# Kernel tuning notes

Hardware: AMD Instinct MI355X
Metric: run time of the kernel (lower is better)

## Reference

```python
import jax, jax.numpy as jnp
import numpy as np

ALPHA = 10.0
BETA = 2.0
NUM_CLASSES = 98
EMB = 512
N = 8192

def l2_normalize(x, axis):
    return x / jnp.linalg.norm(x, axis=axis, keepdims=True)

def setup_inputs() -> dict:
    key = jax.random.key(0)
    k1, k2, k3 = jax.random.split(key, 3)
    inputs = jax.random.normal(k1, (N, EMB), dtype=jnp.float32)
    inputs = l2_normalize(inputs, axis=1)  # embeddings are unit-norm cosine features
    targets = jax.random.randint(k2, (N,), 0, NUM_CLASSES, dtype=jnp.int64)
    # kernel: uniform(-1,1) then renorm columns to tiny norm then scale -> effectively
    # columns get L2-normalized anyway in forward; plain uniform init is faithful.
    kernel = jax.random.uniform(k3, (EMB, NUM_CLASSES), dtype=jnp.float32, minval=-1.0, maxval=1.0)
    return {"inputs": inputs, "targets": targets, "kernel": kernel}

def reference(inputs, targets, kernel):
    n = inputs.shape[0]
    # pairwise similarity [n, n]
    sim_mat = inputs @ inputs.T
    # margin-adjusted logits
    kernel_norm = l2_normalize(kernel, axis=0)
    cos_theta = jnp.clip(inputs @ kernel_norm, -1.0, 1.0)  # [n, C]
    onehot = jax.nn.one_hot(targets, NUM_CLASSES, dtype=jnp.bool_)
    output = jnp.where(onehot, cos_theta - BETA, cos_theta) * ALPHA
    # cross entropy (mean)
    logp = jax.nn.log_softmax(output, axis=1)
    loss = -jnp.mean(jnp.take_along_axis(logp, targets[:, None], axis=1))
    # precision
    pred = jnp.argmax(output, axis=1)
    prec = jnp.mean((pred == targets).astype(jnp.float32))
    # vectorized per-sample masked pos/neg similarity means
    same = targets[:, None] == targets[None, :]           # [n, n]
    pos_mask = same & (sim_mat < 1.0)                     # excludes self (sim == 1)
    neg_mask = ~same
    posf = pos_mask.astype(sim_mat.dtype)
    negf = neg_mask.astype(sim_mat.dtype)
    pos_mean_i = jnp.sum(sim_mat * posf, axis=1) / jnp.sum(posf, axis=1)
    neg_mean_i = jnp.sum(sim_mat * negf, axis=1) / jnp.sum(negf, axis=1)
    mean_pos_sim = jnp.mean(pos_mean_i)
    mean_neg_sim = jnp.mean(neg_mean_i)
    return (loss, prec, mean_pos_sim, mean_neg_sim)
```

## Files before the change

kernel.cpp:

```cpp
#include <hip/hip_runtime.h>
#include <hip/hip_bf16.h>

typedef __attribute__((ext_vector_type(8))) short bf16x8;
typedef __attribute__((ext_vector_type(4))) float f32x4;

#define NROWS 8192
#define EMB   512
#define NCLS  98
#define NCPAD 128
#define MAXPER 256
#define NBLK  (NROWS / 32)
#define ALPHA_F 10.0f
#define BETA_F  2.0f

__device__ __forceinline__ unsigned short f2bf(float x) {
    unsigned u = __builtin_bit_cast(unsigned, x);
    u += 0x7FFF + ((u >> 16) & 1);
    return (unsigned short)(u >> 16);
}

__device__ __forceinline__ void g2l16(const void* g, void* l) {
    __builtin_amdgcn_global_load_lds(
        (const __attribute__((address_space(1))) unsigned int*)g,
        (__attribute__((address_space(3))) unsigned int*)l, 16, 0, 0);
}

__global__ __launch_bounds__(1024) void init_scatter_kernel(
        const int* __restrict__ T, int* __restrict__ cnt, int* __restrict__ bucket,
        unsigned int* __restrict__ ctr, float* __restrict__ usum) {
    __shared__ int lh[NCLS];
    const int tid = threadIdx.x;
    if (tid < NCLS) lh[tid] = 0;
    if (tid == 0) *ctr = 0;
    if (tid < EMB) usum[tid] = 0.f;
    __syncthreads();
    #pragma unroll
    for (int k = 0; k < NROWS / 1024; ++k) {
        int i = k * 1024 + tid;
        int t = T[i];
        int slot = atomicAdd(&lh[t], 1);
        if (slot < MAXPER) bucket[t * MAXPER + slot] = i;
    }
    __syncthreads();
    if (tid < NCLS) cnt[tid] = lh[tid];
}

__global__ __launch_bounds__(256) void classv_kernel(
        const float* __restrict__ X, const float* __restrict__ K,
        const int* __restrict__ cnt, const int* __restrict__ bucket,
        float* __restrict__ V, float* __restrict__ usum,
        unsigned short* __restrict__ KbT) {
    const int tid = threadIdx.x;
    const int lane = tid & 63, w = tid >> 6;
    const int bx = blockIdx.x;

    if (bx >= 784) {
        int c = (bx - 784) * 4 + w;
        if (c < NCLS) {
            float v[8]; float s = 0.f;
            #pragma unroll
            for (int q = 0; q < 8; ++q) {
                float x = K[(size_t)(lane + q * 64) * NCLS + c];
                v[q] = x; s = fmaf(x, x, s);
            }
            #pragma unroll
            for (int d = 32; d > 0; d >>= 1) s += __shfl_xor(s, d);
            float inv = 1.0f / sqrtf(s);
            #pragma unroll
            for (int q = 0; q < 8; ++q)
                KbT[(size_t)c * EMB + lane + q * 64] = f2bf(v[q] * inv);
        } else {
            #pragma unroll
            for (int q = 0; q < 8; ++q)
                KbT[(size_t)c * EMB + lane + q * 64] = 0;
        }
        return;
    }

    __shared__ float red[3][64];
    const int c = bx >> 3, d0 = (bx & 7) * 64;
    int n = cnt[c]; if (n > MAXPER) n = MAXPER;
    const int* bk = bucket + c * MAXPER;
    float a = 0.f;
    for (int j = w; j < n; j += 4) {
        int row = bk[j];
        a += X[(size_t)row * EMB + d0 + lane];
    }
    if (w > 0) red[w - 1][lane] = a;
    __syncthreads();
    if (w == 0) {
        a += red[0][lane] + red[1][lane] + red[2][lane];
        V[(size_t)c * EMB + d0 + lane] = a;
        atomicAdd(&usum[d0 + lane], a);
    }
}

__global__ __launch_bounds__(256) void main_gemm(
        const float* __restrict__ X, const unsigned short* __restrict__ KbT,
        const int* __restrict__ T, const int* __restrict__ cnt,
        const float* __restrict__ V, const float* __restrict__ usum,
        double* __restrict__ partials, unsigned int* __restrict__ ctr,
        float* __restrict__ out) {
    __shared__ unsigned short As[32 * 64];
    __shared__ unsigned short Bs[NCPAD * 64];
    __shared__ float P[32][NCPAD];
    __shared__ int   trow[32];
    __shared__ double redacc[4][4];
    __shared__ int   lastflag;

    const int tid = threadIdx.x;
    const int w = tid >> 6, lane = tid & 63;
    const int row0 = blockIdx.x * 32;
    const int wr = w & 1, wc = w >> 1;
    const int c0 = lane & 15, g = lane >> 4;

    const int ar = tid >> 3, ak = (tid & 7) * 8;
    const int myt = T[row0 + ar];
    if (tid < 32) trow[tid] = T[row0 + tid];
    const float* vrow = V + (size_t)myt * EMB;

    float s = 0.f, sm = 0.f; double d = 0.0;
    f32x4 av[4] = {};
    for (int kk = 0; kk < EMB; kk += 64) {
        const float* xp = X + (size_t)(row0 + ar) * EMB + kk + ak;
        float4 xa0 = *(const float4*)xp, xa1 = *(const float4*)(xp + 4);
        const float* up = usum + kk + ak;
        float4 ua0 = *(const float4*)up, ua1 = *(const float4*)(up + 4);
        const float* vp = vrow + kk + ak;
        float4 va0 = *(const float4*)vp, va1 = *(const float4*)(vp + 4);
        float xf[8] = {xa0.x, xa0.y, xa0.z, xa0.w, xa1.x, xa1.y, xa1.z, xa1.w};
        float uf[8] = {ua0.x, ua0.y, ua0.z, ua0.w, ua1.x, ua1.y, ua1.z, ua1.w};
        float vf[8] = {va0.x, va0.y, va0.z, va0.w, va1.x, va1.y, va1.z, va1.w};
        bf16x8 areg;
        #pragma unroll
        for (int q = 0; q < 8; ++q) {
            s  = fmaf(xf[q], uf[q], s);
            sm = fmaf(xf[q], vf[q], sm);
            d  = fma((double)xf[q], (double)xf[q], d);
            areg[q] = (short)f2bf(xf[q]);
        }
        __syncthreads();
        *(bf16x8*)&As[ar * 64 + ak] = areg;
        #pragma unroll
        for (int q = 0; q < 4; ++q) {
            int lb = q * 4096 + tid * 16;
            int c = lb >> 7, kb = lb & 127;
            g2l16((const char*)KbT + (size_t)c * 1024 + kk * 2 + kb, (char*)Bs + lb);
        }
        __syncthreads();
        #pragma unroll
        for (int ks = 0; ks < 2; ++ks) {
            bf16x8 a = *(const bf16x8*)&As[(wr * 16 + c0) * 64 + ks * 32 + g * 8];
            #pragma unroll
            for (int ni = 0; ni < 4; ++ni) {
                bf16x8 b = *(const bf16x8*)&Bs[(wc * 64 + ni * 16 + c0) * 64 + ks * 32 + g * 8];
                av[ni] = __builtin_amdgcn_mfma_f32_16x16x32_bf16(a, b, av[ni], 0, 0, 0);
            }
        }
    }

    #pragma unroll
    for (int m = 1; m < 8; m <<= 1) {
        s += __shfl_xor(s, m); sm += __shfl_xor(sm, m); d += __shfl_xor(d, m);
    }
    double pc = 0.0, nc = 0.0;
    if ((lane & 7) == 0) {
        int h = cnt[myt];
        float pos_sum; int pos_cnt;
        if (d < 1.0) { pos_sum = sm;            pos_cnt = h;     }
        else         { pos_sum = sm - (float)d; pos_cnt = h - 1; }
        float neg_sum = s - sm;
        pc = (double)(pos_sum / (float)pos_cnt);
        nc = (double)(neg_sum / (float)(NROWS - h));
    }
    #pragma unroll
    for (int m = 1; m < 64; m <<= 1) { pc += __shfl_xor(pc, m); nc += __shfl_xor(nc, m); }

    __syncthreads();
    #pragma unroll
    for (int ni = 0; ni < 4; ++ni)
        #pragma unroll
        for (int r = 0; r < 4; ++r)
            P[wr * 16 + g * 4 + r][wc * 64 + ni * 16 + c0] = av[ni][r];
    __syncthreads();

    float lossacc = 0.f, pracc = 0.f;
    #pragma unroll
    for (int j = 0; j < 8; ++j) {
        const int rl = w * 8 + j;
        const int tgt = trow[rl];
        float l1 = P[rl][lane], l2 = P[rl][lane + 64];
        {
            float cos1 = fminf(1.f, fmaxf(-1.f, l1));
            float cos2 = fminf(1.f, fmaxf(-1.f, l2));
            l1 = (cos1 - (lane == tgt ? BETA_F : 0.f)) * ALPHA_F;
            l2 = (cos2 - (lane + 64 == tgt ? BETA_F : 0.f)) * ALPHA_F;
            if (lane      >= NCLS) l1 = -1e30f;
            if (lane + 64 >= NCLS) l2 = -1e30f;
        }
        float m = fmaxf(l1, l2);
        #pragma unroll
        for (int dd = 1; dd < 64; dd <<= 1) m = fmaxf(m, __shfl_xor(m, dd));
        float se = (lane < NCLS ? __expf(l1 - m) : 0.f)
                 + (lane + 64 < NCLS ? __expf(l2 - m) : 0.f);
        float tval = (lane == tgt) ? l1 : ((lane + 64 == tgt) ? l2 : -1e30f);
        float bv; int bi;
        if (l2 > l1) { bv = l2; bi = lane + 64; } else { bv = l1; bi = lane; }
        #pragma unroll
        for (int dd = 1; dd < 64; dd <<= 1) {
            se += __shfl_xor(se, dd);
            tval = fmaxf(tval, __shfl_xor(tval, dd));
            float ov = __shfl_xor(bv, dd); int oi = __shfl_xor(bi, dd);
            if (ov > bv || (ov == bv && oi < bi)) { bv = ov; bi = oi; }
        }
        lossacc += (m + logf(se)) - tval;
        pracc   += (bi == tgt) ? 1.f : 0.f;
    }

    if (lane == 0) {
        redacc[w][0] = (double)lossacc;
        redacc[w][1] = (double)pracc;
        redacc[w][2] = pc;
        redacc[w][3] = nc;
    }
    __syncthreads();
    if (tid == 0) {
        const int bx = blockIdx.x;
        partials[bx * 4 + 0] = redacc[0][0] + redacc[1][0] + redacc[2][0] + redacc[3][0];
        partials[bx * 4 + 1] = redacc[0][1] + redacc[1][1] + redacc[2][1] + redacc[3][1];
        partials[bx * 4 + 2] = redacc[0][2] + redacc[1][2] + redacc[2][2] + redacc[3][2];
        partials[bx * 4 + 3] = redacc[0][3] + redacc[1][3] + redacc[2][3] + redacc[3][3];
        __threadfence();
        lastflag = (atomicAdd(ctr, 1u) == NBLK - 1) ? 1 : 0;
    }
    __syncthreads();
    if (lastflag && w == 0) {
        __threadfence();
        double a0 = 0.0, a1 = 0.0, a2 = 0.0, a3 = 0.0;
        for (int i = lane; i < NBLK; i += 64) {
            a0 += partials[i * 4 + 0];
            a1 += partials[i * 4 + 1];
            a2 += partials[i * 4 + 2];
            a3 += partials[i * 4 + 3];
        }
        #pragma unroll
        for (int m = 1; m < 64; m <<= 1) {
            a0 += __shfl_xor(a0, m); a1 += __shfl_xor(a1, m);
            a2 += __shfl_xor(a2, m); a3 += __shfl_xor(a3, m);
        }
        if (lane == 0) {
            out[0] = (float)(a0 / NROWS);
            out[1] = (float)(a1 / NROWS);
            out[2] = (float)(a2 / NROWS);
            out[3] = (float)(a3 / NROWS);
        }
    }
}

#define BM 64
#define BN 64
#define BK 32
#define LDA 68

__global__ void hist_kernel(const int* __restrict__ t, int* __restrict__ hist) {
    int i = blockIdx.x * blockDim.x + threadIdx.x;
    if (i < NROWS) atomicAdd(&hist[t[i]], 1);
}

__global__ void colnorm_kernel(const float* __restrict__ K, float* __restrict__ colinv) {
    int c = blockIdx.x;
    float s = 0.f;
    for (int k = threadIdx.x; k < EMB; k += 64) {
        float v = K[k * NCLS + c];
        s = fmaf(v, v, s);
    }
    #pragma unroll
    for (int off = 32; off > 0; off >>= 1) s += __shfl_down(s, off);
    if (threadIdx.x == 0) colinv[c] = 1.0f / sqrtf(s);
}

__global__ __launch_bounds__(256) void simred_kernel(
        const float* __restrict__ X, const int* __restrict__ T,
        float* __restrict__ S, float* __restrict__ SAME) {
    __shared__ float As[BK * LDA];
    __shared__ float Bs[BK * LDA];
    __shared__ int   trow[BM], tcol[BN];
    __shared__ float redS[BM], redSame[BM];

    const int tid = threadIdx.x;
    const int tx = tid & 15, ty = tid >> 4;
    const int i0 = blockIdx.x * BM, j0 = blockIdx.y * BN;

    if (tid < BM) {
        trow[tid] = T[i0 + tid];
        tcol[tid] = T[j0 + tid];
        redS[tid] = 0.f;
        redSame[tid] = 0.f;
    }

    float c[4][4] = {};
    for (int kk = 0; kk < EMB; kk += BK) {
        #pragma unroll
        for (int q = 0; q < 2; ++q) {
            int l  = tid * 2 + q;
            int r  = l >> 3;
            int kq = (l & 7) << 2;
            const float4 va = *(const float4*)(X + (size_t)(i0 + r) * EMB + kk + kq);
            As[(kq + 0) * LDA + r] = va.x;
            As[(kq + 1) * LDA + r] = va.y;
            As[(kq + 2) * LDA + r] = va.z;
            As[(kq + 3) * LDA + r] = va.w;
            const float4 vb = *(const float4*)(X + (size_t)(j0 + r) * EMB + kk + kq);
            Bs[(kq + 0) * LDA + r] = vb.x;
            Bs[(kq + 1) * LDA + r] = vb.y;
            Bs[(kq + 2) * LDA + r] = vb.z;
            Bs[(kq + 3) * LDA + r] = vb.w;
        }
        __syncthreads();
        #pragma unroll
        for (int k = 0; k < BK; ++k) {
            float4 a4 = *(const float4*)&As[k * LDA + ty * 4];
            float4 b4 = *(const float4*)&Bs[k * LDA + tx * 4];
            float a[4] = {a4.x, a4.y, a4.z, a4.w};
            float b[4] = {b4.x, b4.y, b4.z, b4.w};
            #pragma unroll
            for (int i = 0; i < 4; ++i)
                #pragma unroll
                for (int j = 0; j < 4; ++j)
                    c[i][j] = fmaf(a[i], b[j], c[i][j]);
        }
        __syncthreads();
    }

    #pragma unroll
    for (int i = 0; i < 4; ++i) {
        int r = ty * 4 + i;
        int tr = trow[r];
        float s = 0.f, sm = 0.f;
        #pragma unroll
        for (int j = 0; j < 4; ++j) {
            float v = c[i][j];
            s += v;
            if (tcol[tx * 4 + j] == tr) sm += v;
        }
        atomicAdd(&redS[r], s);
        atomicAdd(&redSame[r], sm);
    }
    __syncthreads();
    if (tid < BM) {
        atomicAdd(&S[i0 + tid],    redS[tid]);
        atomicAdd(&SAME[i0 + tid], redSame[tid]);
    }
}

__global__ __launch_bounds__(128) void loss_kernel(
        const float* __restrict__ X, const int* __restrict__ T,
        const float* __restrict__ K, const float* __restrict__ colinv,
        double* __restrict__ acc) {
    const int row = blockIdx.x;
    const int tid = threadIdx.x;
    __shared__ float xs[EMB];
    *(float4*)&xs[tid * 4] = *(const float4*)&X[(size_t)row * EMB + tid * 4];
    __syncthreads();

    const int tgt = T[row];
    const int c = tid;
    float logit = -1e30f;
    if (c < NCLS) {
        float d = 0.f;
        #pragma unroll 4
        for (int k = 0; k < EMB; ++k) d = fmaf(K[k * NCLS + c], xs[k], d);
        float cosv = d * colinv[c];
        cosv = fminf(1.f, fmaxf(-1.f, cosv));
        logit = (cosv - (c == tgt ? BETA_F : 0.f)) * ALPHA_F;
    }

    __shared__ float rv[128];
    __shared__ int   ri[128];
    __shared__ float Lt;
    if (c == tgt) Lt = logit;

    rv[tid] = logit;
    __syncthreads();
    #pragma unroll
    for (int s = 64; s > 0; s >>= 1) {
        if (tid < s) rv[tid] = fmaxf(rv[tid], rv[tid + s]);
        __syncthreads();
    }
    const float m = rv[0];
    __syncthreads();

    rv[tid] = (c < NCLS) ? expf(logit - m) : 0.f;
    __syncthreads();
    #pragma unroll
    for (int s = 64; s > 0; s >>= 1) {
        if (tid < s) rv[tid] += rv[tid + s];
        __syncthreads();
    }
    const float lse = m + logf(rv[0]);
    __syncthreads();

    rv[tid] = logit;
    ri[tid] = (c < NCLS) ? c : 0x7fffffff;
    __syncthreads();
    #pragma unroll
    for (int s = 64; s > 0; s >>= 1) {
        if (tid < s) {
            float vo = rv[tid + s]; int io = ri[tid + s];
            if (vo > rv[tid] || (vo == rv[tid] && io < ri[tid])) { rv[tid] = vo; ri[tid] = io; }
        }
        __syncthreads();
    }

    if (tid == 0) {
        float loss_i = lse - Lt;
        atomicAdd(&acc[0], (double)loss_i);
        atomicAdd(&acc[1], (ri[0] == tgt) ? 1.0 : 0.0);
    }
}

__global__ void finalize_kernel(
        const float* __restrict__ X, const int* __restrict__ T,
        const int* __restrict__ hist, const float* __restrict__ S,
        const float* __restrict__ SAME, double* __restrict__ acc) {
    int r = blockIdx.x * blockDim.x + threadIdx.x;
    if (r >= NROWS) return;
    const float* x = X + (size_t)r * EMB;
    double d = 0.0;
    for (int k = 0; k < EMB; ++k) d = fma((double)x[k], (double)x[k], d);
    int h = hist[T[r]];
    float same = SAME[r];
    float pos_sum; int pos_cnt;
    if (d < 1.0) { pos_sum = same;            pos_cnt = h;     }
    else         { pos_sum = same - (float)d; pos_cnt = h - 1; }
    float neg_sum = S[r] - same;
    int   neg_cnt = NROWS - h;
    atomicAdd(&acc[2], (double)(pos_sum / (float)pos_cnt));
    atomicAdd(&acc[3], (double)(neg_sum / (float)neg_cnt));
}

__global__ void out_kernel(const double* __restrict__ acc, float* __restrict__ out) {
    if (threadIdx.x == 0) {
        out[0] = (float)(acc[0] / NROWS);
        out[1] = (float)(acc[1] / NROWS);
        out[2] = (float)(acc[2] / NROWS);
        out[3] = (float)(acc[3] / NROWS);
    }
}

extern "C" void kernel_launch(void* const* d_in, const int* in_sizes, int n_in,
                              void* d_out, int out_size, void* d_ws, size_t ws_size,
                              hipStream_t stream) {
    const float* X = (const float*)d_in[0];
    const int*   T = (const int*)d_in[1];
    const float* K = (const float*)d_in[2];
    float* out = (float*)d_out;

    const size_t KBT_BYTES    = (size_t)NCPAD * EMB * sizeof(unsigned short);
    const size_t V_BYTES      = (size_t)NCLS * EMB * sizeof(float);
    const size_t BUCKET_BYTES = (size_t)NCLS * MAXPER * sizeof(int);
    const size_t PART_BYTES   = (size_t)NBLK * 4 * sizeof(double);
    const size_t MISC_BYTES   = 128 * sizeof(int) + 64 + 512 * sizeof(float);

    if (ws_size >= KBT_BYTES + V_BYTES + BUCKET_BYTES + PART_BYTES + MISC_BYTES + 256) {
        unsigned short* KbT = (unsigned short*)d_ws;
        float*  V        = (float*)((char*)d_ws + KBT_BYTES);
        int*    bucket   = (int*)((char*)d_ws + KBT_BYTES + V_BYTES);
        double* partials = (double*)((char*)d_ws + KBT_BYTES + V_BYTES + BUCKET_BYTES);
        int*    cnt      = (int*)((char*)partials + PART_BYTES);
        unsigned int* ctr = (unsigned int*)(cnt + 128);
        float*  usum     = (float*)(ctr + 16);

        init_scatter_kernel<<<1, 1024, 0, stream>>>(T, cnt, bucket, ctr, usum);
        classv_kernel<<<816, 256, 0, stream>>>(X, K, cnt, bucket, V, usum, KbT);
        main_gemm<<<NBLK, 256, 0, stream>>>(X, KbT, T, cnt, V, usum, partials, ctr, out);
    } else {
        const size_t FB_BYTES = sizeof(double) * 4 + sizeof(int) * NCLS
                              + sizeof(float) * (NCLS + 2 * NROWS);
        double* acc    = (double*)d_ws;
        int*    hist   = (int*)(acc + 4);
        float*  colinv = (float*)(hist + NCLS);
        float*  S      = colinv + NCLS;
        float*  SAME   = S + NROWS;

        hipMemsetAsync(d_ws, 0, FB_BYTES, stream);
        hist_kernel<<<(NROWS + 255) / 256, 256, 0, stream>>>(T, hist);
        colnorm_kernel<<<NCLS, 64, 0, stream>>>(K, colinv);
        simred_kernel<<<dim3(NROWS / BM, NROWS / BN), 256, 0, stream>>>(X, T, S, SAME);
        loss_kernel<<<NROWS, 128, 0, stream>>>(X, T, K, colinv, acc);
        finalize_kernel<<<(NROWS + 255) / 256, 256, 0, stream>>>(X, T, hist, S, SAME, acc);
        out_kernel<<<1, 64, 0, stream>>>(acc, out);
    }
}
```

Before: 50.18 us.

## Fuse three-kernel pipeline into one cooperative kernel with grid syncs

Replaces the init/scatter, class-vector and main GEMM launches with a single cooperative mega-kernel of 256 blocks that separates its phases with grid.sync(). Init, column normalisation and bucket scatter now run in parallel across blocks instead of in one 1024-thread block. The aim is to remove launch overhead and inter-kernel gaps; in exchange it adds grid-wide barrier costs and relies on cooperative launch, falling back to the old path if that fails. The naive fallback path for a small workspace is removed.

```diff
diff --git a/kernel.cpp b/kernel.cpp
--- a/kernel.cpp
+++ b/kernel.cpp
@@ -1,5 +1,8 @@
 #include <hip/hip_runtime.h>
 #include <hip/hip_bf16.h>
+#include <hip/hip_cooperative_groups.h>
+
+namespace cg = cooperative_groups;
 
 typedef __attribute__((ext_vector_type(8))) short bf16x8;
 typedef __attribute__((ext_vector_type(4))) float f32x4;
@@ -9,7 +12,7 @@
 #define NCLS  98
 #define NCPAD 128
 #define MAXPER 256
-#define NBLK  (NROWS / 32)
+#define NBLK  256
 #define ALPHA_F 10.0f
 #define BETA_F  2.0f
 
@@ -23,6 +26,226 @@
     __builtin_amdgcn_global_load_lds(
         (const __attribute__((address_space(1))) unsigned int*)g,
         (__attribute__((address_space(3))) unsigned int*)l, 16, 0, 0);
+}
+
+__global__ __launch_bounds__(256) void mega_kernel(
+        const float* __restrict__ X, const int* __restrict__ T,
+        const float* __restrict__ K,
+        int* __restrict__ cnt, int* __restrict__ bucket,
+        float* __restrict__ V, float* __restrict__ usum,
+        unsigned short* __restrict__ KbT,
+        double* __restrict__ partials, float* __restrict__ out) {
+    cg::grid_group grid = cg::this_grid();
+
+    __shared__ unsigned short As[32 * 64];
+    __shared__ unsigned short Bs[NCPAD * 64];
+    __shared__ float P[32][NCPAD];
+    __shared__ float redB[3][64];
+    __shared__ int   trow[32];
+    __shared__ double redacc[4][4];
+
+    const int bx = blockIdx.x;
+    const int tid = threadIdx.x;
+    const int w = tid >> 6, lane = tid & 63;
+
+    if (bx == 0) {
+        if (tid < NCLS) cnt[tid] = 0;
+    } else if (bx == 1) {
+        usum[tid] = 0.f; usum[tid + 256] = 0.f;
+    } else if (bx >= 2 && bx < 34) {
+        int c = (bx - 2) * 4 + w;
+        if (c < NCLS) {
+            float v[8]; float s = 0.f;
+            #pragma unroll
+            for (int q = 0; q < 8; ++q) {
+                float x = K[(size_t)(lane + q * 64) * NCLS + c];
+                v[q] = x; s = fmaf(x, x, s);
+            }
+            #pragma unroll
+            for (int d = 32; d > 0; d >>= 1) s += __shfl_xor(s, d);
+            float inv = 1.0f / sqrtf(s);
+            #pragma unroll
+            for (int q = 0; q < 8; ++q)
+                KbT[(size_t)c * EMB + lane + q * 64] = f2bf(v[q] * inv);
+        } else {
+            #pragma unroll
+            for (int q = 0; q < 8; ++q)
+                KbT[(size_t)c * EMB + lane + q * 64] = 0;
+        }
+    }
+    grid.sync();
+
+    if (bx < 32) {
+        int i = bx * 256 + tid;
+        int t = T[i];
+        int slot = atomicAdd(&cnt[t], 1);
+        if (slot < MAXPER) bucket[t * MAXPER + slot] = i;
+    }
+    grid.sync();
+
+    for (int vb = bx; vb < 784; vb += NBLK) {
+        const int c = vb >> 3, d0 = (vb & 7) * 64;
+        int n = cnt[c]; if (n > MAXPER) n = MAXPER;
+        const int* bk = bucket + c * MAXPER;
+        float a = 0.f;
+        for (int j = w; j < n; j += 4) {
+            int row = bk[j];
+            a += X[(size_t)row * EMB + d0 + lane];
+        }
+        if (w > 0) redB[w - 1][lane] = a;
+        __syncthreads();
+        if (w == 0) {
+            a += redB[0][lane] + redB[1][lane] + redB[2][lane];
+            V[(size_t)c * EMB + d0 + lane] = a;
+            atomicAdd(&usum[d0 + lane], a);
+        }
+        __syncthreads();
+    }
+    grid.sync();
+
+    {
+        const int row0 = bx * 32;
+        const int wr = w & 1, wc = w >> 1;
+        const int c0 = lane & 15, g = lane >> 4;
+        const int ar = tid >> 3, ak = (tid & 7) * 8;
+        const int myt = T[row0 + ar];
+        if (tid < 32) trow[tid] = T[row0 + tid];
+        const float* vrow = V + (size_t)myt * EMB;
+
+        float s = 0.f, sm = 0.f; double d = 0.0;
+        f32x4 av[4] = {};
+        for (int kk = 0; kk < EMB; kk += 64) {
+            const float* xp = X + (size_t)(row0 + ar) * EMB + kk + ak;
+            float4 xa0 = *(const float4*)xp, xa1 = *(const float4*)(xp + 4);
+            const float* up = usum + kk + ak;
+            float4 ua0 = *(const float4*)up, ua1 = *(const float4*)(up + 4);
+            const float* vp = vrow + kk + ak;
+            float4 va0 = *(const float4*)vp, va1 = *(const float4*)(vp + 4);
+            float xf[8] = {xa0.x, xa0.y, xa0.z, xa0.w, xa1.x, xa1.y, xa1.z, xa1.w};
+            float uf[8] = {ua0.x, ua0.y, ua0.z, ua0.w, ua1.x, ua1.y, ua1.z, ua1.w};
+            float vf[8] = {va0.x, va0.y, va0.z, va0.w, va1.x, va1.y, va1.z, va1.w};
+            bf16x8 areg;
+            #pragma unroll
+            for (int q = 0; q < 8; ++q) {
+                s  = fmaf(xf[q], uf[q], s);
+                sm = fmaf(xf[q], vf[q], sm);
+                d  = fma((double)xf[q], (double)xf[q], d);
+                areg[q] = (short)f2bf(xf[q]);
+            }
+            __syncthreads();
+            *(bf16x8*)&As[ar * 64 + ak] = areg;
+            #pragma unroll
+            for (int q = 0; q < 4; ++q) {
+                int lb = q * 4096 + tid * 16;
+                int c = lb >> 7, kb = lb & 127;
+                g2l16((const char*)KbT + (size_t)c * 1024 + kk * 2 + kb, (char*)Bs + lb);
+            }
+            __syncthreads();
+            #pragma unroll
+            for (int ks = 0; ks < 2; ++ks) {
+                bf16x8 a = *(const bf16x8*)&As[(wr * 16 + c0) * 64 + ks * 32 + g * 8];
+                #pragma unroll
+                for (int ni = 0; ni < 4; ++ni) {
+                    bf16x8 b = *(const bf16x8*)&Bs[(wc * 64 + ni * 16 + c0) * 64 + ks * 32 + g * 8];
+                    av[ni] = __builtin_amdgcn_mfma_f32_16x16x32_bf16(a, b, av[ni], 0, 0, 0);
+                }
+            }
+        }
+
+        #pragma unroll
+        for (int m = 1; m < 8; m <<= 1) {
+            s += __shfl_xor(s, m); sm += __shfl_xor(sm, m); d += __shfl_xor(d, m);
+        }
+        double pc = 0.0, nc = 0.0;
+        if ((lane & 7) == 0) {
+            int h = cnt[myt];
+            float pos_sum; int pos_cnt;
+            if (d < 1.0) { pos_sum = sm;            pos_cnt = h;     }
+            else         { pos_sum = sm - (float)d; pos_cnt = h - 1; }
+            float neg_sum = s - sm;
+            pc = (double)(pos_sum / (float)pos_cnt);
+            nc = (double)(neg_sum / (float)(NROWS - h));
+        }
+        #pragma unroll
+        for (int m = 1; m < 64; m <<= 1) { pc += __shfl_xor(pc, m); nc += __shfl_xor(nc, m); }
+
+        __syncthreads();
+        #pragma unroll
+        for (int ni = 0; ni < 4; ++ni)
+            #pragma unroll
+            for (int r = 0; r < 4; ++r)
+                P[wr * 16 + g * 4 + r][wc * 64 + ni * 16 + c0] = av[ni][r];
+        __syncthreads();
+
+        float lossacc = 0.f, pracc = 0.f;
+        #pragma unroll
+        for (int j = 0; j < 8; ++j) {
+            const int rl = w * 8 + j;
+            const int tgt = trow[rl];
+            float l1 = P[rl][lane], l2 = P[rl][lane + 64];
+            {
+                float cos1 = fminf(1.f, fmaxf(-1.f, l1));
+                float cos2 = fminf(1.f, fmaxf(-1.f, l2));
+                l1 = (cos1 - (lane == tgt ? BETA_F : 0.f)) * ALPHA_F;
+                l2 = (cos2 - (lane + 64 == tgt ? BETA_F : 0.f)) * ALPHA_F;
+                if (lane      >= NCLS) l1 = -1e30f;
+                if (lane + 64 >= NCLS) l2 = -1e30f;
+            }
+            float m = fmaxf(l1, l2);
+            #pragma unroll
+            for (int dd = 1; dd < 64; dd <<= 1) m = fmaxf(m, __shfl_xor(m, dd));
+            float se = (lane < NCLS ? __expf(l1 - m) : 0.f)
+                     + (lane + 64 < NCLS ? __expf(l2 - m) : 0.f);
+            float tval = (lane == tgt) ? l1 : ((lane + 64 == tgt) ? l2 : -1e30f);
+            float bv; int bi;
+            if (l2 > l1) { bv = l2; bi = lane + 64; } else { bv = l1; bi = lane; }
+            #pragma unroll
+            for (int dd = 1; dd < 64; dd <<= 1) {
+                se += __shfl_xor(se, dd);
+                tval = fmaxf(tval, __shfl_xor(tval, dd));
+                float ov = __shfl_xor(bv, dd); int oi = __shfl_xor(bi, dd);
+                if (ov > bv || (ov == bv && oi < bi)) { bv = ov; bi = oi; }
+            }
+            lossacc += (m + logf(se)) - tval;
+            pracc   += (bi == tgt) ? 1.f : 0.f;
+        }
+
+        if (lane == 0) {
+            redacc[w][0] = (double)lossacc;
+            redacc[w][1] = (double)pracc;
+            redacc[w][2] = pc;
+            redacc[w][3] = nc;
+        }
+        __syncthreads();
+        if (tid == 0) {
+            partials[bx * 4 + 0] = redacc[0][0] + redacc[1][0] + redacc[2][0] + redacc[3][0];
+            partials[bx * 4 + 1] = redacc[0][1] + redacc[1][1] + redacc[2][1] + redacc[3][1];
+            partials[bx * 4 + 2] = redacc[0][2] + redacc[1][2] + redacc[2][2] + redacc[3][2];
+            partials[bx * 4 + 3] = redacc[0][3] + redacc[1][3] + redacc[2][3] + redacc[3][3];
+        }
+    }
+    grid.sync();
+
+    if (bx == 0 && w == 0) {
+        double a0 = 0.0, a1 = 0.0, a2 = 0.0, a3 = 0.0;
+        for (int i = lane; i < NBLK; i += 64) {
+            a0 += partials[i * 4 + 0];
+            a1 += partials[i * 4 + 1];
+            a2 += partials[i * 4 + 2];
+            a3 += partials[i * 4 + 3];
+        }
+        #pragma unroll
+        for (int m = 1; m < 64; m <<= 1) {
+            a0 += __shfl_xor(a0, m); a1 += __shfl_xor(a1, m);
+            a2 += __shfl_xor(a2, m); a3 += __shfl_xor(a3, m);
+        }
+        if (lane == 0) {
+            out[0] = (float)(a0 / NROWS);
+            out[1] = (float)(a1 / NROWS);
+            out[2] = (float)(a2 / NROWS);
+            out[3] = (float)(a3 / NROWS);
+        }
+    }
 }
 
 __global__ __launch_bounds__(1024) void init_scatter_kernel(
@@ -257,197 +480,6 @@
     }
 }
 
-#define BM 64
-#define BN 64
-#define BK 32
-#define LDA 68
-
-__global__ void hist_kernel(const int* __restrict__ t, int* __restrict__ hist) {
-    int i = blockIdx.x * blockDim.x + threadIdx.x;
-    if (i < NROWS) atomicAdd(&hist[t[i]], 1);
-}
-
-__global__ void colnorm_kernel(const float* __restrict__ K, float* __restrict__ colinv) {
-    int c = blockIdx.x;
-    float s = 0.f;
-    for (int k = threadIdx.x; k < EMB; k += 64) {
-        float v = K[k * NCLS + c];
-        s = fmaf(v, v, s);
-    }
-    #pragma unroll
-    for (int off = 32; off > 0; off >>= 1) s += __shfl_down(s, off);
-    if (threadIdx.x == 0) colinv[c] = 1.0f / sqrtf(s);
-}
-
-__global__ __launch_bounds__(256) void simred_kernel(
-        const float* __restrict__ X, const int* __restrict__ T,
-        float* __restrict__ S, float* __restrict__ SAME) {
-    __shared__ float As[BK * LDA];
-    __shared__ float Bs[BK * LDA];
-    __shared__ int   trow[BM], tcol[BN];
-    __shared__ float redS[BM], redSame[BM];
-
-    const int tid = threadIdx.x;
-    const int tx = tid & 15, ty = tid >> 4;
-    const int i0 = blockIdx.x * BM, j0 = blockIdx.y * BN;
-
-    if (tid < BM) {
-        trow[tid] = T[i0 + tid];
-        tcol[tid] = T[j0 + tid];
-        redS[tid] = 0.f;
-        redSame[tid] = 0.f;
-    }
-
-    float c[4][4] = {};
-    for (int kk = 0; kk < EMB; kk += BK) {
-        #pragma unroll
-        for (int q = 0; q < 2; ++q) {
-            int l  = tid * 2 + q;
-            int r  = l >> 3;
-            int kq = (l & 7) << 2;
-            const float4 va = *(const float4*)(X + (size_t)(i0 + r) * EMB + kk + kq);
-            As[(kq + 0) * LDA + r] = va.x;
-            As[(kq + 1) * LDA + r] = va.y;
-            As[(kq + 2) * LDA + r] = va.z;
-            As[(kq + 3) * LDA + r] = va.w;
-            const float4 vb = *(const float4*)(X + (size_t)(j0 + r) * EMB + kk + kq);
-            Bs[(kq + 0) * LDA + r] = vb.x;
-            Bs[(kq + 1) * LDA + r] = vb.y;
-            Bs[(kq + 2) * LDA + r] = vb.z;
-            Bs[(kq + 3) * LDA + r] = vb.w;
-        }
-        __syncthreads();
-        #pragma unroll
-        for (int k = 0; k < BK; ++k) {
-            float4 a4 = *(const float4*)&As[k * LDA + ty * 4];
-            float4 b4 = *(const float4*)&Bs[k * LDA + tx * 4];
-            float a[4] = {a4.x, a4.y, a4.z, a4.w};
-            float b[4] = {b4.x, b4.y, b4.z, b4.w};
-            #pragma unroll
-            for (int i = 0; i < 4; ++i)
-                #pragma unroll
-                for (int j = 0; j < 4; ++j)
-                    c[i][j] = fmaf(a[i], b[j], c[i][j]);
-        }
-        __syncthreads();
-    }
-
-    #pragma unroll
-    for (int i = 0; i < 4; ++i) {
-        int r = ty * 4 + i;
-        int tr = trow[r];
-        float s = 0.f, sm = 0.f;
-        #pragma unroll
-        for (int j = 0; j < 4; ++j) {
-            float v = c[i][j];
-            s += v;
-            if (tcol[tx * 4 + j] == tr) sm += v;
-        }
-        atomicAdd(&redS[r], s);
-        atomicAdd(&redSame[r], sm);
-    }
-    __syncthreads();
-    if (tid < BM) {
-        atomicAdd(&S[i0 + tid],    redS[tid]);
-        atomicAdd(&SAME[i0 + tid], redSame[tid]);
-    }
-}
-
-__global__ __launch_bounds__(128) void loss_kernel(
-        const float* __restrict__ X, const int* __restrict__ T,
-        const float* __restrict__ K, const float* __restrict__ colinv,
-        double* __restrict__ acc) {
-    const int row = blockIdx.x;
-    const int tid = threadIdx.x;
-    __shared__ float xs[EMB];
-    *(float4*)&xs[tid * 4] = *(const float4*)&X[(size_t)row * EMB + tid * 4];
-    __syncthreads();
-
-    const int tgt = T[row];
-    const int c = tid;
-    float logit = -1e30f;
-    if (c < NCLS) {
-        float d = 0.f;
-        #pragma unroll 4
-        for (int k = 0; k < EMB; ++k) d = fmaf(K[k * NCLS + c], xs[k], d);
-        float cosv = d * colinv[c];
-        cosv = fminf(1.f, fmaxf(-1.f, cosv));
-        logit = (cosv - (c == tgt ? BETA_F : 0.f)) * ALPHA_F;
-    }
-
-    __shared__ float rv[128];
-    __shared__ int   ri[128];
-    __shared__ float Lt;
-    if (c == tgt) Lt = logit;
-
-    rv[tid] = logit;
-    __syncthreads();
-    #pragma unroll
-    for (int s = 64; s > 0; s >>= 1) {
-        if (tid < s) rv[tid] = fmaxf(rv[tid], rv[tid + s]);
-        __syncthreads();
-    }
-    const float m = rv[0];
-    __syncthreads();
-
-    rv[tid] = (c < NCLS) ? expf(logit - m) : 0.f;
-    __syncthreads();
-    #pragma unroll
-    for (int s = 64; s > 0; s >>= 1) {
-        if (tid < s) rv[tid] += rv[tid + s];
-        __syncthreads();
-    }
-    const float lse = m + logf(rv[0]);
-    __syncthreads();
-
-    rv[tid] = logit;
-    ri[tid] = (c < NCLS) ? c : 0x7fffffff;
-    __syncthreads();
-    #pragma unroll
-    for (int s = 64; s > 0; s >>= 1) {
-        if (tid < s) {
-            float vo = rv[tid + s]; int io = ri[tid + s];
-            if (vo > rv[tid] || (vo == rv[tid] && io < ri[tid])) { rv[tid] = vo; ri[tid] = io; }
-        }
-        __syncthreads();
-    }
-
-    if (tid == 0) {
-        float loss_i = lse - Lt;
-        atomicAdd(&acc[0], (double)loss_i);
-        atomicAdd(&acc[1], (ri[0] == tgt) ? 1.0 : 0.0);
-    }
-}
-
-__global__ void finalize_kernel(
-        const float* __restrict__ X, const int* __restrict__ T,
-        const int* __restrict__ hist, const float* __restrict__ S,
-        const float* __restrict__ SAME, double* __restrict__ acc) {
-    int r = blockIdx.x * blockDim.x + threadIdx.x;
-    if (r >= NROWS) return;
-    const float* x = X + (size_t)r * EMB;
-    double d = 0.0;
-    for (int k = 0; k < EMB; ++k) d = fma((double)x[k], (double)x[k], d);
-    int h = hist[T[r]];
-    float same = SAME[r];
-    float pos_sum; int pos_cnt;
-    if (d < 1.0) { pos_sum = same;            pos_cnt = h;     }
-    else         { pos_sum = same - (float)d; pos_cnt = h - 1; }
-    float neg_sum = S[r] - same;
-    int   neg_cnt = NROWS - h;
-    atomicAdd(&acc[2], (double)(pos_sum / (float)pos_cnt));
-    atomicAdd(&acc[3], (double)(neg_sum / (float)neg_cnt));
-}
-
-__global__ void out_kernel(const double* __restrict__ acc, float* __restrict__ out) {
-    if (threadIdx.x == 0) {
-        out[0] = (float)(acc[0] / NROWS);
-        out[1] = (float)(acc[1] / NROWS);
-        out[2] = (float)(acc[2] / NROWS);
-        out[3] = (float)(acc[3] / NROWS);
-    }
-}
-
 extern "C" void kernel_launch(void* const* d_in, const int* in_sizes, int n_in,
                               void* d_out, int out_size, void* d_ws, size_t ws_size,
                               hipStream_t stream) {
@@ -462,33 +494,23 @@
     const size_t PART_BYTES   = (size_t)NBLK * 4 * sizeof(double);
     const size_t MISC_BYTES   = 128 * sizeof(int) + 64 + 512 * sizeof(float);
 
-    if (ws_size >= KBT_BYTES + V_BYTES + BUCKET_BYTES + PART_BYTES + MISC_BYTES + 256) {
-        unsigned short* KbT = (unsigned short*)d_ws;
-        float*  V        = (float*)((char*)d_ws + KBT_BYTES);
-        int*    bucket   = (int*)((char*)d_ws + KBT_BYTES + V_BYTES);
-        double* partials = (double*)((char*)d_ws + KBT_BYTES + V_BYTES + BUCKET_BYTES);
-        int*    cnt      = (int*)((char*)partials + PART_BYTES);
-        unsigned int* ctr = (unsigned int*)(cnt + 128);
-        float*  usum     = (float*)(ctr + 16);
-
+    unsigned short* KbT = (unsigned short*)d_ws;
+    float*  V        = (float*)((char*)d_ws + KBT_BYTES);
+    int*    bucket   = (int*)((char*)d_ws + KBT_BYTES + V_BYTES);
+    double* partials = (double*)((char*)d_ws + KBT_BYTES + V_BYTES + BUCKET_BYTES);
+    int*    cnt      = (int*)((char*)partials + PART_BYTES);
+    unsigned int* ctr = (unsigned int*)(cnt + 128);
+    float*  usum     = (float*)(ctr + 16);
+
+    const float* Xa = X; const int* Ta = T; const float* Ka = K;
+    void* args[] = { (void*)&Xa, (void*)&Ta, (void*)&Ka,
+                     (void*)&cnt, (void*)&bucket, (void*)&V, (void*)&usum,
+                     (void*)&KbT, (void*)&partials, (void*)&out };
+    hipError_t err = hipLaunchCooperativeKernel(
+        (const void*)mega_kernel, dim3(NBLK), dim3(256), args, 0, stream);
+    if (err != hipSuccess) {
         init_scatter_kernel<<<1, 1024, 0, stream>>>(T, cnt, bucket, ctr, usum);
         classv_kernel<<<816, 256, 0, stream>>>(X, K, cnt, bucket, V, usum, KbT);
         main_gemm<<<NBLK, 256, 0, stream>>>(X, KbT, T, cnt, V, usum, partials, ctr, out);
-    } else {
-        const size_t FB_BYTES = sizeof(double) * 4 + sizeof(int) * NCLS
-                              + sizeof(float) * (NCLS + 2 * NROWS);
-        double* acc    = (double*)d_ws;
-        int*    hist   = (int*)(acc + 4);
-        float*  colinv = (float*)(hist + NCLS);
-        float*  S      = colinv + NCLS;
-        float*  SAME   = S + NROWS;
-
-        hipMemsetAsync(d_ws, 0, FB_BYTES, stream);
-        hist_kernel<<<(NROWS + 255) / 256, 256, 0, stream>>>(T, hist);
-        colnorm_kernel<<<NCLS, 64, 0, stream>>>(K, colinv);
-        simred_kernel<<<dim3(NROWS / BM, NROWS / BN), 256, 0, stream>>>(X, T, S, SAME);
-        loss_kernel<<<NROWS, 128, 0, stream>>>(X, T, K, colinv, acc);
-        finalize_kernel<<<(NROWS + 255) / 256, 256, 0, stream>>>(X, T, hist, S, SAME, acc);
-        out_kernel<<<1, 64, 0, stream>>>(acc, out);
-    }
-}
+    }
+}
```

New measurement: 171.4 us. +241.5%, slower.
